# Kernel tuning notes

Hardware: AMD Instinct MI355X
Metric: run time of the kernel (lower is better)

Reference implementation:

```python
import jax, jax.numpy as jnp
import numpy as np

B, L, D, H = 65536, 20, 4, 1024
T = 61  # output_length; 60 RK4 steps


def setup_inputs() -> dict:
    key = jax.random.key(0)
    ks = jax.random.split(key, 16)
    # small positive states so the quadratic SEIR dynamics stay finite over 60 steps
    xx = jax.random.uniform(ks[0], (B, L, D), dtype=jnp.float32) * 0.1
    dims = [L * D] + [H] * 6 + [3]
    inp = {"xx": xx}
    for i in range(7):
        scale = 1.0 / np.sqrt(dims[i])
        W = jax.random.normal(ks[1 + 2 * i], (dims[i], dims[i + 1]), dtype=jnp.float32) * scale
        if i == 6:
            W = W * 1e-3  # keep beta/gamma/sigma small -> stable integration
        inp[f"W{i}"] = W
        inp[f"b{i}"] = jnp.zeros((dims[i + 1],), jnp.float32)
    inp["output_length"] = T
    return inp


def reference(xx, W0, b0, W1, b1, W2, b2, W3, b3, W4, b4, W5, b5, W6, b6, output_length):
    h = xx.reshape(xx.shape[0], -1)  # (B, L*D)
    for W, b in ((W0, b0), (W1, b1), (W2, b2), (W3, b3), (W4, b4), (W5, b5)):
        h = jax.nn.leaky_relu(h @ W + b, negative_slope=0.01)
    out = h @ W6 + b6  # (B, 3)
    beta, gamma, sigma = out[:, 0:1], out[:, 1:2], out[:, 2:3]  # each (B,1)

    initial = xx[:, 0]  # (B, 4) = S,E,I,R at t0
    S0, E0, I0, R0 = (initial[:, i:i + 1] for i in range(4))
    # self.step = 1 in the torch module, so dt is folded in as 1.0

    def derivs(S, E, I):
        SI = beta * S * I
        return -SI, SI - sigma * E, sigma * E - gamma * I, gamma * I

    def body(carry, _):
        S, E, I, R = carry
        k1S, k1E, k1I, k1R = derivs(S, E, I)
        k2S, k2E, k2I, k2R = derivs(S + 0.5 * k1S, E + 0.5 * k1E, I + 0.5 * k1I)
        k3S, k3E, k3I, k3R = derivs(S + 0.5 * k2S, E + 0.5 * k2E, I + 0.5 * k2I)
        k4S, k4E, k4I, k4R = derivs(S + k3S, E + k3E, I + k3I)
        upd = lambda f, k1, k2, k3, k4: f + (k1 + 2 * k2 + 2 * k3 + k4) / 6.0
        new = (upd(S, k1S, k2S, k3S, k4S),
               upd(E, k1E, k2E, k3E, k4E),
               upd(I, k1I, k2I, k3I, k4I),
               upd(R, k1R, k2R, k3R, k4R))
        return new, jnp.concatenate(new, axis=1)  # (B,4) per step

    _, ys = jax.lax.scan(body, (S0, E0, I0, R0), None, length=output_length - 1)
    y0 = jnp.concatenate([S0, E0, I0, R0], axis=1)  # (B,4)
    y = jnp.concatenate([y0[None], ys], axis=0)     # (T,B,4)
    return jnp.transpose(y, (1, 0, 2))              # (B,T,4) in S,E,I,R order
```

## Files before the change

kernel.cpp:

```cpp
#include <hip/hip_runtime.h>
#include <stdint.h>

typedef short s16x8 __attribute__((ext_vector_type(8)));
typedef __bf16 bf16x8 __attribute__((ext_vector_type(8)));
typedef float f32x4 __attribute__((ext_vector_type(4)));

typedef const __attribute__((address_space(1))) void* gas_ptr;
typedef __attribute__((address_space(3))) void* las_ptr;

__device__ __forceinline__ unsigned short f2bf(float f) {
  unsigned u = __builtin_bit_cast(unsigned, f);
  u += 0x7FFFu + ((u >> 16) & 1u);
  return (unsigned short)(u >> 16);
}
__device__ __forceinline__ float bf2f(unsigned short h) {
  return __builtin_bit_cast(float, (unsigned)h << 16);
}
__device__ __forceinline__ void async16(const void* g, void* l) {
  __builtin_amdgcn_global_load_lds((gas_ptr)g, (las_ptr)l, 16, 0, 0);
}

__global__ void prep_x0(const float* __restrict__ xx, unsigned short* __restrict__ X0,
                        int rowOffset, int rows) {
  int idx = blockIdx.x * blockDim.x + threadIdx.x;
  if (idx >= rows * 128) return;
  int r = idx >> 7, c = idx & 127;
  float v = (c < 80) ? xx[(size_t)(rowOffset + r) * 80 + c] : 0.f;
  X0[(size_t)r * 128 + c] = f2bf(v);
}

struct TP {
  const float* W[6];
  unsigned short* WT[6];
  const float* xx;
  unsigned short* X0;
  int prepRows;
};

__global__ void prep_all(TP tp) {
  const int z = blockIdx.z;
  const int tx = threadIdx.x, ty = threadIdx.y;
  if (z == 6) {
    const long long total = (long long)tp.prepRows * 128;
    long long i = ((long long)(blockIdx.y * 32 + blockIdx.x) * 256) + (ty * 32 + tx);
    for (; i < total; i += 262144) {
      const int r = (int)(i >> 7), c = (int)(i & 127);
      float v = (c < 80) ? tp.xx[(size_t)r * 80 + c] : 0.f;
      tp.X0[(size_t)r * 128 + c] = f2bf(v);
    }
    return;
  }
  const int K  = (z == 0) ? 80  : 1024;
  const int KP = (z == 0) ? 128 : 1024;
  if (blockIdx.y * 32 >= KP) return;
  __shared__ float tile[32][33];
  const int n0 = blockIdx.x * 32, k0 = blockIdx.y * 32;
  const float* W = tp.W[z];
  unsigned short* WT = tp.WT[z];
  #pragma unroll
  for (int j = 0; j < 32; j += 8) {
    int k = k0 + ty + j;
    tile[ty + j][tx] = (k < K) ? W[(size_t)k * 1024 + n0 + tx] : 0.f;
  }
  __syncthreads();
  #pragma unroll
  for (int j = 0; j < 32; j += 8) {
    WT[(size_t)(n0 + ty + j) * KP + k0 + tx] = f2bf(tile[tx][ty + j]);
  }
}

#define BM 128
#define BN 128
#define BK 64

__global__ void gemm_mlp(const unsigned short* __restrict__ A,
                         const unsigned short* __restrict__ BT,
                         const float* __restrict__ bias,
                         unsigned short* __restrict__ C,
                         int M, int N, int K, int leaky) {
  __shared__ unsigned short As[BM * BK];
  __shared__ unsigned short Bs[BN * BK];

  const int tid  = threadIdx.x;
  const int wid  = tid >> 6;
  const int lane = tid & 63;
  const int wr = (wid >> 1) * 64;
  const int wc = (wid & 1) * 64;
  const int bn = blockIdx.x * BN;
  const int bm = blockIdx.y * BM;

  const int srow = lane >> 3;
  const int scol = (lane & 7) * 8;

  f32x4 acc[4][4] = {};

  const unsigned short* aTile = A  + (size_t)bm * K;
  const unsigned short* bTile = BT + (size_t)bn * K;

  for (int k0 = 0; k0 < K; k0 += BK) {
    #pragma unroll
    for (int j = 0; j < 4; ++j) {
      const int rg = wid + j * 4;
      async16(aTile + (size_t)(rg * 8 + srow) * K + k0 + scol, &As[rg * 8 * BK]);
      async16(bTile + (size_t)(rg * 8 + srow) * K + k0 + scol, &Bs[rg * 8 * BK]);
    }
    __syncthreads();

    const int fr = lane & 15;
    const int kq = (lane >> 4) * 8;
    #pragma unroll
    for (int ks = 0; ks < BK; ks += 32) {
      const int kk = ks + kq;
      bf16x8 af[4], bv[4];
      #pragma unroll
      for (int m = 0; m < 4; ++m)
        af[m] = __builtin_bit_cast(bf16x8, *(const s16x8*)&As[(wr + m * 16 + fr) * BK + kk]);
      #pragma unroll
      for (int n = 0; n < 4; ++n)
        bv[n] = __builtin_bit_cast(bf16x8, *(const s16x8*)&Bs[(wc + n * 16 + fr) * BK + kk]);
      #pragma unroll
      for (int m = 0; m < 4; ++m)
        #pragma unroll
        for (int n = 0; n < 4; ++n)
          acc[m][n] = __builtin_amdgcn_mfma_f32_16x16x32_bf16(af[m], bv[n], acc[m][n], 0, 0, 0);
    }
    __syncthreads();
  }

  const int fcol = lane & 15;
  const int frow = (lane >> 4) * 4;
  #pragma unroll
  for (int m = 0; m < 4; ++m) {
    #pragma unroll
    for (int n = 0; n < 4; ++n) {
      const int col = bn + wc + n * 16 + fcol;
      const float bb = bias[col];
      #pragma unroll
      for (int r = 0; r < 4; ++r) {
        const int row = bm + wr + m * 16 + frow + r;
        float v = acc[m][n][r] + bb;
        if (leaky) v = (v > 0.f) ? v : 0.01f * v;
        C[(size_t)row * N + col] = f2bf(v);
      }
    }
  }
}


__device__ __forceinline__ void stage_half(const char* srcRow0, size_t ldb,
                                           char* ldsHalf, int w, int rsub, int usw) {
  #pragma unroll
  for (int l = 0; l < 2; ++l) {
    const char* src = srcRow0 + (size_t)((l * 8 + w) * 8 + rsub) * ldb + usw;
    async16(src, ldsHalf + (l * 8 + w) * 1024);
  }
}

#define MFMA16 __builtin_amdgcn_mfma_f32_16x16x32_bf16
#define EPAD 72
#define EBYTES (64 * EPAD * 2)

template <int HEAD>
__global__ __launch_bounds__(512, 2)
void gemm8(const unsigned short* __restrict__ A,
           const unsigned short* __restrict__ BT,
           const float* __restrict__ bias,
           unsigned short* __restrict__ C,
           const float* __restrict__ W6,
           float* __restrict__ partial,
           int M, int N, int K) {
  extern __shared__ char smem[];
  char* smA = smem;
  char* smB = smem + 65536;
  const unsigned short* sA = (const unsigned short*)smA;
  const unsigned short* sB = (const unsigned short*)smB;
  const int NTk = K >> 6;

  const int tid  = threadIdx.x;
  const int w    = tid >> 6;
  const int lane = tid & 63;

  const int nwg = gridDim.x;
  const int bid = blockIdx.x;
  const int q = nwg >> 3, r = nwg & 7;
  const int xcd = bid & 7, idx = bid >> 3;
  const int wg = (xcd < r ? xcd * (q + 1) : r * (q + 1) + (xcd - r) * q) + idx;
  const int nNT = N >> 8;
  const int mtile = wg / nNT, ntile = wg % nNT;
  const int bm = mtile << 8, bn = ntile << 8;

  const int wr = (w >> 2) << 7;
  const int wc = (w & 3) << 6;
  const int fr = lane & 15;
  const int e0 = lane >> 4;
  const int sw = lane & 7;
  const int rsub = lane >> 3;
  const int usw  = ((sw ^ rsub) << 4);
  const int col0 = (((e0)     ^ sw) << 3);
  const int col1 = (((e0 + 4) ^ sw) << 3);
  const int fcol = lane & 15;

  const size_t ldb = (size_t)K * 2;
  const char* Ab = (const char*)A  + (size_t)bm * ldb;
  const char* Bb = (const char*)BT + (size_t)bn * ldb;

  f32x4 acc[8][4] = {};

#define RDA(c_, row_, col_) __builtin_bit_cast(bf16x8, *(const s16x8*)&sA[(c_) * 16384 + (row_) * 64 + (col_)])
#define RDB(c_, row_, col_) __builtin_bit_cast(bf16x8, *(const s16x8*)&sB[(c_) * 16384 + (row_) * 64 + (col_)])

  stage_half(Bb,                    ldb, smB,                  w, rsub, usw);
  stage_half(Bb + 128 * ldb,        ldb, smB + 16384,          w, rsub, usw);
  stage_half(Ab,                    ldb, smA,                  w, rsub, usw);
  stage_half(Ab + 128 * ldb,        ldb, smA + 16384,          w, rsub, usw);
  stage_half(Bb + 128,              ldb, smB + 32768,          w, rsub, usw);
  stage_half(Bb + 128 * ldb + 128,  ldb, smB + 32768 + 16384,  w, rsub, usw);
  asm volatile("s_waitcnt vmcnt(4)" ::: "memory");
  __builtin_amdgcn_s_barrier();

  for (int kt = 0; kt < NTk; ++kt) {
    const int c = kt & 1;
    bf16x8 aF[4][2], bF[4][2];

    #pragma unroll
    for (int m = 0; m < 4; ++m) {
      const int row = wr + m * 16 + fr;
      aF[m][0] = RDA(c, row, col0);
      aF[m][1] = RDA(c, row, col1);
    }
    #pragma unroll
    for (int n = 0; n < 2; ++n) {
      const int row = wc + n * 16 + fr;
      bF[n][0] = RDB(c, row, col0);
      bF[n][1] = RDB(c, row, col1);
    }
    if (kt + 1 < NTk)
      stage_half(Ab + (size_t)(kt + 1) * 128, ldb, smA + (c ^ 1) * 32768, w, rsub, usw);
    __builtin_amdgcn_s_barrier();
    __builtin_amdgcn_s_setprio(1);
    #pragma unroll
    for (int m = 0; m < 4; ++m)
      #pragma unroll
      for (int n = 0; n < 2; ++n) {
        acc[m][n] = MFMA16(aF[m][0], bF[n][0], acc[m][n], 0, 0, 0);
        acc[m][n] = MFMA16(aF[m][1], bF[n][1], acc[m][n], 0, 0, 0);
      }
    __builtin_amdgcn_s_setprio(0);
    __builtin_amdgcn_s_barrier();

    #pragma unroll
    for (int n = 2; n < 4; ++n) {
      const int row = wc + n * 16 + fr;
      bF[n][0] = RDB(c, row, col0);
      bF[n][1] = RDB(c, row, col1);
    }
    if (kt + 1 < NTk)
      stage_half(Ab + 128 * ldb + (size_t)(kt + 1) * 128, ldb,
                 smA + (c ^ 1) * 32768 + 16384, w, rsub, usw);
    __builtin_amdgcn_s_barrier();
    __builtin_amdgcn_s_setprio(1);
    #pragma unroll
    for (int m = 0; m < 4; ++m)
      #pragma unroll
      for (int n = 2; n < 4; ++n) {
        acc[m][n] = MFMA16(aF[m][0], bF[n][0], acc[m][n], 0, 0, 0);
        acc[m][n] = MFMA16(aF[m][1], bF[n][1], acc[m][n], 0, 0, 0);
      }
    __builtin_amdgcn_s_setprio(0);
    __builtin_amdgcn_s_barrier();

    #pragma unroll
    for (int m = 0; m < 4; ++m) {
      const int row = wr + (m + 4) * 16 + fr;
      aF[m][0] = RDA(c, row, col0);
      aF[m][1] = RDA(c, row, col1);
    }
    if (kt + 2 < NTk)
      stage_half(Bb + (size_t)(kt + 2) * 128, ldb, smB + c * 32768, w, rsub, usw);
    __builtin_amdgcn_s_barrier();
    __builtin_amdgcn_s_setprio(1);
    #pragma unroll
    for (int m = 0; m < 4; ++m)
      #pragma unroll
      for (int n = 0; n < 2; ++n) {
        acc[m + 4][n] = MFMA16(aF[m][0], bF[n][0], acc[m + 4][n], 0, 0, 0);
        acc[m + 4][n] = MFMA16(aF[m][1], bF[n][1], acc[m + 4][n], 0, 0, 0);
      }
    __builtin_amdgcn_s_setprio(0);
    __builtin_amdgcn_s_barrier();

    if (kt + 2 < NTk)
      stage_half(Bb + 128 * ldb + (size_t)(kt + 2) * 128, ldb,
                 smB + c * 32768 + 16384, w, rsub, usw);
    __builtin_amdgcn_s_barrier();
    __builtin_amdgcn_s_setprio(1);
    #pragma unroll
    for (int m = 0; m < 4; ++m)
      #pragma unroll
      for (int n = 2; n < 4; ++n) {
        acc[m + 4][n] = MFMA16(aF[m][0], bF[n][0], acc[m + 4][n], 0, 0, 0);
        acc[m + 4][n] = MFMA16(aF[m][1], bF[n][1], acc[m + 4][n], 0, 0, 0);
      }
    __builtin_amdgcn_s_setprio(0);
    if (kt + 2 < NTk) asm volatile("s_waitcnt vmcnt(4)" ::: "memory");
    else              asm volatile("s_waitcnt vmcnt(0)" ::: "memory");
    __builtin_amdgcn_s_barrier();
  }

#undef RDA
#undef RDB

  float bbv[4];
  #pragma unroll
  for (int n = 0; n < 4; ++n) bbv[n] = bias[bn + wc + n * 16 + fcol];

  if constexpr (HEAD) {
    float w6c[4][3];
    #pragma unroll
    for (int n = 0; n < 4; ++n) {
      const int col = bn + wc + n * 16 + fcol;
      #pragma unroll
      for (int j = 0; j < 3; ++j) w6c[n][j] = W6[col * 3 + j];
    }
    const int nt = bn >> 8;
    #pragma unroll
    for (int mh = 0; mh < 2; ++mh)
      #pragma unroll
      for (int mm = 0; mm < 4; ++mm)
        #pragma unroll
        for (int rr = 0; rr < 4; ++rr) {
          float s0 = 0.f, s1 = 0.f, s2 = 0.f;
          #pragma unroll
          for (int n = 0; n < 4; ++n) {
            float v = acc[mh * 4 + mm][n][rr] + bbv[n];
            v = (v > 0.f) ? v : 0.01f * v;
            s0 = fmaf(v, w6c[n][0], s0);
            s1 = fmaf(v, w6c[n][1], s1);
            s2 = fmaf(v, w6c[n][2], s2);
          }
          #pragma unroll
          for (int off = 1; off < 16; off <<= 1) {
            s0 += __shfl_xor(s0, off);
            s1 += __shfl_xor(s1, off);
            s2 += __shfl_xor(s2, off);
          }
          if (fcol == 0) {
            const int row = bm + wr + mh * 64 + mm * 16 + e0 * 4 + rr;
            *(float4*)&partial[((size_t)nt * M + row) * 4] =
                make_float4(s0, s1, s2, 0.f);
          }
        }
  } else {
    unsigned short* eb = (unsigned short*)(smem + w * EBYTES);
    const int r8 = lane >> 3, c8 = (lane & 7) * 8;
    #pragma unroll
    for (int mh = 0; mh < 2; ++mh) {
      #pragma unroll
      for (int mm = 0; mm < 4; ++mm)
        #pragma unroll
        for (int n = 0; n < 4; ++n)
          #pragma unroll
          for (int rr = 0; rr < 4; ++rr) {
            const int row64 = mm * 16 + e0 * 4 + rr;
            float v = acc[mh * 4 + mm][n][rr] + bbv[n];
            v = (v > 0.f) ? v : 0.01f * v;
            eb[row64 * EPAD + n * 16 + fcol] = f2bf(v);
          }
      asm volatile("" ::: "memory");
      #pragma unroll
      for (int rg = 0; rg < 8; ++rg) {
        const int row64 = rg * 8 + r8;
        s16x8 vv = *(const s16x8*)&eb[row64 * EPAD + c8];
        const int rl = bm + wr + mh * 64 + row64;
        *(s16x8*)&C[(size_t)rl * N + bn + wc + c8] = vv;
      }
      asm volatile("" ::: "memory");
    }
  }
}

__global__ void rk4_traj(const float* __restrict__ partial,
                         const float* __restrict__ b6,
                         const float* __restrict__ xx,
                         float* __restrict__ out,
                         int rowOffset, int rows, int T) {
  const int r = blockIdx.x * blockDim.x + threadIdx.x;
  if (r >= rows) return;
  const size_t grow = (size_t)rowOffset + r;

  float4 p0 = *(const float4*)&partial[((size_t)0 * rows + r) * 4];
  float4 p1 = *(const float4*)&partial[((size_t)1 * rows + r) * 4];
  float4 p2 = *(const float4*)&partial[((size_t)2 * rows + r) * 4];
  float4 p3 = *(const float4*)&partial[((size_t)3 * rows + r) * 4];
  const float beta  = p0.x + p1.x + p2.x + p3.x + b6[0];
  const float gamma = p0.y + p1.y + p2.y + p3.y + b6[1];
  const float sigma = p0.z + p1.z + p2.z + p3.z + b6[2];

  const float4 iv = *(const float4*)(xx + grow * 80);
  float S = iv.x, E = iv.y, I = iv.z, R = iv.w;
  float* o = out + grow * (size_t)T * 4;
  *(float4*)o = iv;

#define DERIVS(S_, E_, I_, dS, dE, dI, dR)      \
  {                                             \
    float SI = beta * (S_) * (I_);              \
    float sE = sigma * (E_);                    \
    float gI = gamma * (I_);                    \
    dS = -SI; dE = SI - sE; dI = sE - gI; dR = gI; \
  }

  for (int t = 1; t < T; ++t) {
    float k1S, k1E, k1I, k1R; DERIVS(S, E, I, k1S, k1E, k1I, k1R);
    float k2S, k2E, k2I, k2R; DERIVS(S + 0.5f * k1S, E + 0.5f * k1E, I + 0.5f * k1I, k2S, k2E, k2I, k2R);
    float k3S, k3E, k3I, k3R; DERIVS(S + 0.5f * k2S, E + 0.5f * k2E, I + 0.5f * k2I, k3S, k3E, k3I, k3R);
    float k4S, k4E, k4I, k4R; DERIVS(S + k3S, E + k3E, I + k3I, k4S, k4E, k4I, k4R);
    S += (k1S + 2.f * k2S + 2.f * k3S + k4S) * (1.f / 6.f);
    E += (k1E + 2.f * k2E + 2.f * k3E + k4E) * (1.f / 6.f);
    I += (k1I + 2.f * k2I + 2.f * k3I + k4I) * (1.f / 6.f);
    R += (k1R + 2.f * k2R + 2.f * k3R + k4R) * (1.f / 6.f);
    *(float4*)(o + (size_t)t * 4) = make_float4(S, E, I, R);
  }
#undef DERIVS
}

extern "C" void kernel_launch(void* const* d_in, const int* in_sizes, int n_in,
                              void* d_out, int out_size, void* d_ws, size_t ws_size,
                              hipStream_t stream) {
  const float* xx = (const float*)d_in[0];
  const float* W[7];
  const float* bb[7];
  for (int i = 0; i < 7; ++i) {
    W[i]  = (const float*)d_in[1 + 2 * i];
    bb[i] = (const float*)d_in[2 + 2 * i];
  }
  const int B = in_sizes[0] / 80;
  const int T = out_size / (B * 4);
  float* out = (float*)d_out;

  {
    auto k0 = gemm8<0>;
    auto k1 = gemm8<1>;
    hipFuncSetAttribute((const void*)k0, hipFuncAttributeMaxDynamicSharedMemorySize, 131072);
    hipFuncSetAttribute((const void*)k1, hipFuncAttributeMaxDynamicSharedMemorySize, 131072);
  }

  uint8_t* ws = (uint8_t*)d_ws;
  size_t off = 0;
  auto alloc = [&](size_t bytes) -> uint8_t* {
    uint8_t* p = ws + off;
    off += (bytes + 255) & ~(size_t)255;
    return p;
  };

  unsigned short* WTl[6];
  WTl[0] = (unsigned short*)alloc((size_t)1024 * 128 * 2);
  for (int i = 1; i < 6; ++i) WTl[i] = (unsigned short*)alloc((size_t)1024 * 1024 * 2);

  const size_t weightBytes = off;
  const size_t avail = ws_size > weightBytes ? ws_size - weightBytes : 0;
  int Bc = (int)(avail / 4416);
  Bc = (Bc / 256) * 256;
  if (Bc > B) Bc = B;
  if (Bc < 256) Bc = 256;
  const bool fullBatch = (Bc >= B);

  unsigned short* X0   = (unsigned short*)alloc((size_t)Bc * 128 * 2);
  unsigned short* buf0 = (unsigned short*)alloc((size_t)Bc * 1024 * 2);
  unsigned short* buf1 = (unsigned short*)alloc((size_t)Bc * 1024 * 2);
  float* partial       = (float*)alloc((size_t)Bc * 4 * 16);

  {
    TP tp;
    for (int i = 0; i < 6; ++i) { tp.W[i] = W[i]; tp.WT[i] = WTl[i]; }
    tp.xx = xx;
    tp.X0 = X0;
    tp.prepRows = fullBatch ? B : 0;
    prep_all<<<dim3(32, 32, 7), dim3(32, 8), 0, stream>>>(tp);
  }

  for (int r0 = 0; r0 < B; r0 += Bc) {
    const int rows = (B - r0 < Bc) ? (B - r0) : Bc;

    if (!fullBatch) {
      const int n = rows * 128;
      prep_x0<<<(n + 255) / 256, 256, 0, stream>>>(xx, X0, r0, rows);
    }

    gemm_mlp<<<dim3(8, rows / 128), 256, 0, stream>>>(X0, WTl[0], bb[0], buf0,
                                                      rows, 1024, 128, 1);

    const int nwg = (rows / 256) * 4;
    gemm8<0><<<nwg, 512, 131072, stream>>>(buf0, WTl[1], bb[1], buf1, nullptr, nullptr, rows, 1024, 1024);
    gemm8<0><<<nwg, 512, 131072, stream>>>(buf1, WTl[2], bb[2], buf0, nullptr, nullptr, rows, 1024, 1024);
    gemm8<0><<<nwg, 512, 131072, stream>>>(buf0, WTl[3], bb[3], buf1, nullptr, nullptr, rows, 1024, 1024);
    gemm8<0><<<nwg, 512, 131072, stream>>>(buf1, WTl[4], bb[4], buf0, nullptr, nullptr, rows, 1024, 1024);

    gemm8<1><<<nwg, 512, 131072, stream>>>(buf0, WTl[5], bb[5], nullptr, W[6], partial, rows, 1024, 1024);

    rk4_traj<<<(rows + 255) / 256, 256, 0, stream>>>(partial, bb[6], xx, out, r0, rows, T);
  }
}
```

Measured before the change: 963.6 us.

## Fuse RK4 trajectory into last GEMM via atomic last-block counter

Removes the separate rk4_traj kernel. Each M-tile in the final layer's GEMM bumps an atomic counter, and the last of the four N-tile workgroups to finish sums the partials and runs the RK4 integration in-kernel. This saves a kernel launch and the partial-buffer round trip, and lets the integration overlap with other GEMM tiles. The cost is atomic synchronisation and RK4 work on only 256 of 512 threads in the finishing block, with a counter reset per tile.

After: 1.038 ms. 7.7% more time.

```diff
diff --git a/kernel.cpp b/kernel.cpp
--- a/kernel.cpp
+++ b/kernel.cpp
@@ -34,6 +34,7 @@
   unsigned short* WT[6];
   const float* xx;
   unsigned short* X0;
+  unsigned* cnt;
   int prepRows;
 };
 
@@ -41,6 +42,10 @@
   const int z = blockIdx.z;
   const int tx = threadIdx.x, ty = threadIdx.y;
   if (z == 6) {
+    if (blockIdx.x == 0 && blockIdx.y == 0) {
+      const int t = ty * 32 + tx;
+      if (t < 256) tp.cnt[t] = 0;
+    }
     const long long total = (long long)tp.prepRows * 128;
     long long i = ((long long)(blockIdx.y * 32 + blockIdx.x) * 256) + (ty * 32 + tx);
     for (; i < total; i += 262144) {
@@ -168,6 +173,11 @@
            unsigned short* __restrict__ C,
            const float* __restrict__ W6,
            float* __restrict__ partial,
+           unsigned* __restrict__ cnt,
+           const float* __restrict__ xx,
+           const float* __restrict__ b6,
+           float* __restrict__ out,
+           int rowOffset, int T,
            int M, int N, int K) {
   extern __shared__ char smem[];
   char* smA = smem;
@@ -346,10 +356,59 @@
           }
           if (fcol == 0) {
             const int row = bm + wr + mh * 64 + mm * 16 + e0 * 4 + rr;
-            *(float4*)&partial[((size_t)nt * M + row) * 4] =
-                make_float4(s0, s1, s2, 0.f);
+            float* p = &partial[((size_t)nt * M + row) * 4];
+            __hip_atomic_store(p + 0, s0, __ATOMIC_RELAXED, __HIP_MEMORY_SCOPE_AGENT);
+            __hip_atomic_store(p + 1, s1, __ATOMIC_RELAXED, __HIP_MEMORY_SCOPE_AGENT);
+            __hip_atomic_store(p + 2, s2, __ATOMIC_RELAXED, __HIP_MEMORY_SCOPE_AGENT);
           }
         }
+
+    __syncthreads();
+    unsigned* sh = (unsigned*)smem;
+    if (tid == 0)
+      sh[0] = __hip_atomic_fetch_add(&cnt[mtile], 1u, __ATOMIC_ACQ_REL,
+                                     __HIP_MEMORY_SCOPE_AGENT);
+    __syncthreads();
+    if (sh[0] == 3u) {
+      if (tid < 256) {
+        const int row = bm + tid;
+        float pv0 = 0.f, pv1 = 0.f, pv2 = 0.f;
+        #pragma unroll
+        for (int nt2 = 0; nt2 < 4; ++nt2) {
+          const float* p = &partial[((size_t)nt2 * M + row) * 4];
+          pv0 += __hip_atomic_load(p + 0, __ATOMIC_RELAXED, __HIP_MEMORY_SCOPE_AGENT);
+          pv1 += __hip_atomic_load(p + 1, __ATOMIC_RELAXED, __HIP_MEMORY_SCOPE_AGENT);
+          pv2 += __hip_atomic_load(p + 2, __ATOMIC_RELAXED, __HIP_MEMORY_SCOPE_AGENT);
+        }
+        const float beta = pv0 + b6[0], gamma = pv1 + b6[1], sigma = pv2 + b6[2];
+        const size_t grow = (size_t)rowOffset + row;
+        const float4 iv = *(const float4*)(xx + grow * 80);
+        float S = iv.x, E = iv.y, I = iv.z, R = iv.w;
+        float* o = out + grow * (size_t)T * 4;
+        *(float4*)o = iv;
+#define DERIVS(S_, E_, I_, dS, dE, dI, dR)         \
+        {                                          \
+          float SI = beta * (S_) * (I_);           \
+          float sE = sigma * (E_);                 \
+          float gI = gamma * (I_);                 \
+          dS = -SI; dE = SI - sE; dI = sE - gI; dR = gI; \
+        }
+        for (int t = 1; t < T; ++t) {
+          float k1S, k1E, k1I, k1R; DERIVS(S, E, I, k1S, k1E, k1I, k1R);
+          float k2S, k2E, k2I, k2R; DERIVS(S + 0.5f * k1S, E + 0.5f * k1E, I + 0.5f * k1I, k2S, k2E, k2I, k2R);
+          float k3S, k3E, k3I, k3R; DERIVS(S + 0.5f * k2S, E + 0.5f * k2E, I + 0.5f * k2I, k3S, k3E, k3I, k3R);
+          float k4S, k4E, k4I, k4R; DERIVS(S + k3S, E + k3E, I + k3I, k4S, k4E, k4I, k4R);
+          S += (k1S + 2.f * k2S + 2.f * k3S + k4S) * (1.f / 6.f);
+          E += (k1E + 2.f * k2E + 2.f * k3E + k4E) * (1.f / 6.f);
+          I += (k1I + 2.f * k2I + 2.f * k3I + k4I) * (1.f / 6.f);
+          R += (k1R + 2.f * k2R + 2.f * k3R + k4R) * (1.f / 6.f);
+          *(float4*)(o + (size_t)t * 4) = make_float4(S, E, I, R);
+        }
+#undef DERIVS
+      }
+      if (tid == 0)
+        __hip_atomic_store(&cnt[mtile], 0u, __ATOMIC_RELAXED, __HIP_MEMORY_SCOPE_AGENT);
+    }
   } else {
     unsigned short* eb = (unsigned short*)(smem + w * EBYTES);
     const int r8 = lane >> 3, c8 = (lane & 7) * 8;
@@ -379,50 +438,6 @@
   }
 }
 
-__global__ void rk4_traj(const float* __restrict__ partial,
-                         const float* __restrict__ b6,
-                         const float* __restrict__ xx,
-                         float* __restrict__ out,
-                         int rowOffset, int rows, int T) {
-  const int r = blockIdx.x * blockDim.x + threadIdx.x;
-  if (r >= rows) return;
-  const size_t grow = (size_t)rowOffset + r;
-
-  float4 p0 = *(const float4*)&partial[((size_t)0 * rows + r) * 4];
-  float4 p1 = *(const float4*)&partial[((size_t)1 * rows + r) * 4];
-  float4 p2 = *(const float4*)&partial[((size_t)2 * rows + r) * 4];
-  float4 p3 = *(const float4*)&partial[((size_t)3 * rows + r) * 4];
-  const float beta  = p0.x + p1.x + p2.x + p3.x + b6[0];
-  const float gamma = p0.y + p1.y + p2.y + p3.y + b6[1];
-  const float sigma = p0.z + p1.z + p2.z + p3.z + b6[2];
-
-  const float4 iv = *(const float4*)(xx + grow * 80);
-  float S = iv.x, E = iv.y, I = iv.z, R = iv.w;
-  float* o = out + grow * (size_t)T * 4;
-  *(float4*)o = iv;
-
-#define DERIVS(S_, E_, I_, dS, dE, dI, dR)      \
-  {                                             \
-    float SI = beta * (S_) * (I_);              \
-    float sE = sigma * (E_);                    \
-    float gI = gamma * (I_);                    \
-    dS = -SI; dE = SI - sE; dI = sE - gI; dR = gI; \
-  }
-
-  for (int t = 1; t < T; ++t) {
-    float k1S, k1E, k1I, k1R; DERIVS(S, E, I, k1S, k1E, k1I, k1R);
-    float k2S, k2E, k2I, k2R; DERIVS(S + 0.5f * k1S, E + 0.5f * k1E, I + 0.5f * k1I, k2S, k2E, k2I, k2R);
-    float k3S, k3E, k3I, k3R; DERIVS(S + 0.5f * k2S, E + 0.5f * k2E, I + 0.5f * k2I, k3S, k3E, k3I, k3R);
-    float k4S, k4E, k4I, k4R; DERIVS(S + k3S, E + k3E, I + k3I, k4S, k4E, k4I, k4R);
-    S += (k1S + 2.f * k2S + 2.f * k3S + k4S) * (1.f / 6.f);
-    E += (k1E + 2.f * k2E + 2.f * k3E + k4E) * (1.f / 6.f);
-    I += (k1I + 2.f * k2I + 2.f * k3I + k4I) * (1.f / 6.f);
-    R += (k1R + 2.f * k2R + 2.f * k3R + k4R) * (1.f / 6.f);
-    *(float4*)(o + (size_t)t * 4) = make_float4(S, E, I, R);
-  }
-#undef DERIVS
-}
-
 extern "C" void kernel_launch(void* const* d_in, const int* in_sizes, int n_in,
                               void* d_out, int out_size, void* d_ws, size_t ws_size,
                               hipStream_t stream) {
@@ -455,6 +470,7 @@
   unsigned short* WTl[6];
   WTl[0] = (unsigned short*)alloc((size_t)1024 * 128 * 2);
   for (int i = 1; i < 6; ++i) WTl[i] = (unsigned short*)alloc((size_t)1024 * 1024 * 2);
+  unsigned* cnt = (unsigned*)alloc(256 * sizeof(unsigned));
 
   const size_t weightBytes = off;
   const size_t avail = ws_size > weightBytes ? ws_size - weightBytes : 0;
@@ -474,6 +490,7 @@
     for (int i = 0; i < 6; ++i) { tp.W[i] = W[i]; tp.WT[i] = WTl[i]; }
     tp.xx = xx;
     tp.X0 = X0;
+    tp.cnt = cnt;
     tp.prepRows = fullBatch ? B : 0;
     prep_all<<<dim3(32, 32, 7), dim3(32, 8), 0, stream>>>(tp);
   }
@@ -490,13 +507,21 @@
                                                       rows, 1024, 128, 1);
 
     const int nwg = (rows / 256) * 4;
-    gemm8<0><<<nwg, 512, 131072, stream>>>(buf0, WTl[1], bb[1], buf1, nullptr, nullptr, rows, 1024, 1024);
-    gemm8<0><<<nwg, 512, 131072, stream>>>(buf1, WTl[2], bb[2], buf0, nullptr, nullptr, rows, 1024, 1024);
-    gemm8<0><<<nwg, 512, 131072, stream>>>(buf0, WTl[3], bb[3], buf1, nullptr, nullptr, rows, 1024, 1024);
-    gemm8<0><<<nwg, 512, 131072, stream>>>(buf1, WTl[4], bb[4], buf0, nullptr, nullptr, rows, 1024, 1024);
-
-    gemm8<1><<<nwg, 512, 131072, stream>>>(buf0, WTl[5], bb[5], nullptr, W[6], partial, rows, 1024, 1024);
-
-    rk4_traj<<<(rows + 255) / 256, 256, 0, stream>>>(partial, bb[6], xx, out, r0, rows, T);
-  }
-}
+    gemm8<0><<<nwg, 512, 131072, stream>>>(buf0, WTl[1], bb[1], buf1, nullptr, nullptr,
+                                           nullptr, nullptr, nullptr, nullptr, 0, 0,
+                                           rows, 1024, 1024);
+    gemm8<0><<<nwg, 512, 131072, stream>>>(buf1, WTl[2], bb[2], buf0, nullptr, nullptr,
+                                           nullptr, nullptr, nullptr, nullptr, 0, 0,
+                                           rows, 1024, 1024);
+    gemm8<0><<<nwg, 512, 131072, stream>>>(buf0, WTl[3], bb[3], buf1, nullptr, nullptr,
+                                           nullptr, nullptr, nullptr, nullptr, 0, 0,
+                                           rows, 1024, 1024);
+    gemm8<0><<<nwg, 512, 131072, stream>>>(buf1, WTl[4], bb[4], buf0, nullptr, nullptr,
+                                           nullptr, nullptr, nullptr, nullptr, 0, 0,
+                                           rows, 1024, 1024);
+
+    gemm8<1><<<nwg, 512, 131072, stream>>>(buf0, WTl[5], bb[5], nullptr, W[6], partial,
+                                           cnt, xx, bb[6], out, r0, T,
+                                           rows, 1024, 1024);
+  }
+}
```

## Fuse final MLP layer, output head and RK4 integration into one kernel

Applied to the files above, without the earlier changes.

Replaces the templated head GEMM plus separate rk4_traj kernel with a gemm8_head kernel where each workgroup owns a 256-row M tile and loops over all four N tiles. The 3-wide head partial sums go into extra LDS, are reduced per row, and the RK4 trajectory is integrated and written out in the same kernel. This removes the global partial buffer and one launch. The cost is that the last GEMM launches a quarter as many workgroups, each doing four times the work, so parallelism and occupancy on that layer drop (extra LDS also raises per-block shared memory).

After: 1.066 ms. 1.11x slower.

```diff
diff --git a/kernel.cpp b/kernel.cpp
--- a/kernel.cpp
+++ b/kernel.cpp
@@ -160,14 +160,108 @@
 #define EPAD 72
 #define EBYTES (64 * EPAD * 2)
 
-template <int HEAD>
+#define GEMM8_KLOOP                                                              \
+  stage_half(Bb,                    ldb, smB,                  w, rsub, usw);    \
+  stage_half(Bb + 128 * ldb,        ldb, smB + 16384,          w, rsub, usw);    \
+  stage_half(Ab,                    ldb, smA,                  w, rsub, usw);    \
+  stage_half(Ab + 128 * ldb,        ldb, smA + 16384,          w, rsub, usw);    \
+  stage_half(Bb + 128,              ldb, smB + 32768,          w, rsub, usw);    \
+  stage_half(Bb + 128 * ldb + 128,  ldb, smB + 32768 + 16384,  w, rsub, usw);    \
+  asm volatile("s_waitcnt vmcnt(4)" ::: "memory");                               \
+  __builtin_amdgcn_s_barrier();                                                  \
+  for (int kt = 0; kt < NTk; ++kt) {                                             \
+    const int c = kt & 1;                                                        \
+    bf16x8 aF[4][2], bF[4][2];                                                   \
+    _Pragma("unroll")                                                            \
+    for (int m = 0; m < 4; ++m) {                                                \
+      const int row = wr + m * 16 + fr;                                          \
+      aF[m][0] = RDA(c, row, col0);                                              \
+      aF[m][1] = RDA(c, row, col1);                                              \
+    }                                                                            \
+    _Pragma("unroll")                                                            \
+    for (int n = 0; n < 2; ++n) {                                                \
+      const int row = wc + n * 16 + fr;                                          \
+      bF[n][0] = RDB(c, row, col0);                                              \
+      bF[n][1] = RDB(c, row, col1);                                              \
+    }                                                                            \
+    if (kt + 1 < NTk)                                                            \
+      stage_half(Ab + (size_t)(kt + 1) * 128, ldb, smA + (c ^ 1) * 32768, w, rsub, usw); \
+    __builtin_amdgcn_s_barrier();                                                \
+    __builtin_amdgcn_s_setprio(1);                                               \
+    _Pragma("unroll")                                                            \
+    for (int m = 0; m < 4; ++m)                                                  \
+      _Pragma("unroll")                                                          \
+      for (int n = 0; n < 2; ++n) {                                              \
+        acc[m][n] = MFMA16(aF[m][0], bF[n][0], acc[m][n], 0, 0, 0);              \
+        acc[m][n] = MFMA16(aF[m][1], bF[n][1], acc[m][n], 0, 0, 0);              \
+      }                                                                          \
+    __builtin_amdgcn_s_setprio(0);                                               \
+    __builtin_amdgcn_s_barrier();                                                \
+    _Pragma("unroll")                                                            \
+    for (int n = 2; n < 4; ++n) {                                                \
+      const int row = wc + n * 16 + fr;                                          \
+      bF[n][0] = RDB(c, row, col0);                                              \
+      bF[n][1] = RDB(c, row, col1);                                              \
+    }                                                                            \
+    if (kt + 1 < NTk)                                                            \
+      stage_half(Ab + 128 * ldb + (size_t)(kt + 1) * 128, ldb,                   \
+                 smA + (c ^ 1) * 32768 + 16384, w, rsub, usw);                   \
+    __builtin_amdgcn_s_barrier();                                                \
+    __builtin_amdgcn_s_setprio(1);                                               \
+    _Pragma("unroll")                                                            \
+    for (int m = 0; m < 4; ++m)                                                  \
+      _Pragma("unroll")                                                          \
+      for (int n = 2; n < 4; ++n) {                                              \
+        acc[m][n] = MFMA16(aF[m][0], bF[n][0], acc[m][n], 0, 0, 0);              \
+        acc[m][n] = MFMA16(aF[m][1], bF[n][1], acc[m][n], 0, 0, 0);              \
+      }                                                                          \
+    __builtin_amdgcn_s_setprio(0);                                               \
+    __builtin_amdgcn_s_barrier();                                                \
+    _Pragma("unroll")                                                            \
+    for (int m = 0; m < 4; ++m) {                                                \
+      const int row = wr + (m + 4) * 16 + fr;                                    \
+      aF[m][0] = RDA(c, row, col0);                                              \
+      aF[m][1] = RDA(c, row, col1);                                              \
+    }                                                                            \
+    if (kt + 2 < NTk)                                                            \
+      stage_half(Bb + (size_t)(kt + 2) * 128, ldb, smB + c * 32768, w, rsub, usw); \
+    __builtin_amdgcn_s_barrier();                                                \
+    __builtin_amdgcn_s_setprio(1);                                               \
+    _Pragma("unroll")                                                            \
+    for (int m = 0; m < 4; ++m)                                                  \
+      _Pragma("unroll")                                                          \
+      for (int n = 0; n < 2; ++n) {                                              \
+        acc[m + 4][n] = MFMA16(aF[m][0], bF[n][0], acc[m + 4][n], 0, 0, 0);      \
+        acc[m + 4][n] = MFMA16(aF[m][1], bF[n][1], acc[m + 4][n], 0, 0, 0);      \
+      }                                                                          \
+    __builtin_amdgcn_s_setprio(0);                                               \
+    __builtin_amdgcn_s_barrier();                                                \
+    if (kt + 2 < NTk)                                                            \
+      stage_half(Bb + 128 * ldb + (size_t)(kt + 2) * 128, ldb,                   \
+                 smB + c * 32768 + 16384, w, rsub, usw);                         \
+    __builtin_amdgcn_s_barrier();                                                \
+    __builtin_amdgcn_s_setprio(1);                                               \
+    _Pragma("unroll")                                                            \
+    for (int m = 0; m < 4; ++m)                                                  \
+      _Pragma("unroll")                                                          \
+      for (int n = 2; n < 4; ++n) {                                              \
+        acc[m + 4][n] = MFMA16(aF[m][0], bF[n][0], acc[m + 4][n], 0, 0, 0);      \
+        acc[m + 4][n] = MFMA16(aF[m][1], bF[n][1], acc[m + 4][n], 0, 0, 0);      \
+      }                                                                          \
+    __builtin_amdgcn_s_setprio(0);                                               \
+    if (kt + 2 < NTk) asm volatile("s_waitcnt vmcnt(4)" ::: "memory");           \
+    else              asm volatile("s_waitcnt vmcnt(0)" ::: "memory");           \
+    __builtin_amdgcn_s_barrier();                                                \
+  }
+
+#define RDA(c_, row_, col_) __builtin_bit_cast(bf16x8, *(const s16x8*)&sA[(c_) * 16384 + (row_) * 64 + (col_)])
+#define RDB(c_, row_, col_) __builtin_bit_cast(bf16x8, *(const s16x8*)&sB[(c_) * 16384 + (row_) * 64 + (col_)])
+
 __global__ __launch_bounds__(512, 2)
 void gemm8(const unsigned short* __restrict__ A,
            const unsigned short* __restrict__ BT,
            const float* __restrict__ bias,
            unsigned short* __restrict__ C,
-           const float* __restrict__ W6,
-           float* __restrict__ partial,
            int M, int N, int K) {
   extern __shared__ char smem[];
   char* smA = smem;
@@ -206,123 +300,100 @@
 
   f32x4 acc[8][4] = {};
 
-#define RDA(c_, row_, col_) __builtin_bit_cast(bf16x8, *(const s16x8*)&sA[(c_) * 16384 + (row_) * 64 + (col_)])
-#define RDB(c_, row_, col_) __builtin_bit_cast(bf16x8, *(const s16x8*)&sB[(c_) * 16384 + (row_) * 64 + (col_)])
-
-  stage_half(Bb,                    ldb, smB,                  w, rsub, usw);
-  stage_half(Bb + 128 * ldb,        ldb, smB + 16384,          w, rsub, usw);
-  stage_half(Ab,                    ldb, smA,                  w, rsub, usw);
-  stage_half(Ab + 128 * ldb,        ldb, smA + 16384,          w, rsub, usw);
-  stage_half(Bb + 128,              ldb, smB + 32768,          w, rsub, usw);
-  stage_half(Bb + 128 * ldb + 128,  ldb, smB + 32768 + 16384,  w, rsub, usw);
-  asm volatile("s_waitcnt vmcnt(4)" ::: "memory");
-  __builtin_amdgcn_s_barrier();
-
-  for (int kt = 0; kt < NTk; ++kt) {
-    const int c = kt & 1;
-    bf16x8 aF[4][2], bF[4][2];
-
-    #pragma unroll
-    for (int m = 0; m < 4; ++m) {
-      const int row = wr + m * 16 + fr;
-      aF[m][0] = RDA(c, row, col0);
-      aF[m][1] = RDA(c, row, col1);
-    }
-    #pragma unroll
-    for (int n = 0; n < 2; ++n) {
-      const int row = wc + n * 16 + fr;
-      bF[n][0] = RDB(c, row, col0);
-      bF[n][1] = RDB(c, row, col1);
-    }
-    if (kt + 1 < NTk)
-      stage_half(Ab + (size_t)(kt + 1) * 128, ldb, smA + (c ^ 1) * 32768, w, rsub, usw);
-    __builtin_amdgcn_s_barrier();
-    __builtin_amdgcn_s_setprio(1);
-    #pragma unroll
-    for (int m = 0; m < 4; ++m)
-      #pragma unroll
-      for (int n = 0; n < 2; ++n) {
-        acc[m][n] = MFMA16(aF[m][0], bF[n][0], acc[m][n], 0, 0, 0);
-        acc[m][n] = MFMA16(aF[m][1], bF[n][1], acc[m][n], 0, 0, 0);
-      }
-    __builtin_amdgcn_s_setprio(0);
-    __builtin_amdgcn_s_barrier();
-
-    #pragma unroll
-    for (int n = 2; n < 4; ++n) {
-      const int row = wc + n * 16 + fr;
-      bF[n][0] = RDB(c, row, col0);
-      bF[n][1] = RDB(c, row, col1);
-    }
-    if (kt + 1 < NTk)
-      stage_half(Ab + 128 * ldb + (size_t)(kt + 1) * 128, ldb,
-                 smA + (c ^ 1) * 32768 + 16384, w, rsub, usw);
-    __builtin_amdgcn_s_barrier();
-    __builtin_amdgcn_s_setprio(1);
-    #pragma unroll
-    for (int m = 0; m < 4; ++m)
-      #pragma unroll
-      for (int n = 2; n < 4; ++n) {
-        acc[m][n] = MFMA16(aF[m][0], bF[n][0], acc[m][n], 0, 0, 0);
-        acc[m][n] = MFMA16(aF[m][1], bF[n][1], acc[m][n], 0, 0, 0);
-      }
-    __builtin_amdgcn_s_setprio(0);
-    __builtin_amdgcn_s_barrier();
-
-    #pragma unroll
-    for (int m = 0; m < 4; ++m) {
-      const int row = wr + (m + 4) * 16 + fr;
-      aF[m][0] = RDA(c, row, col0);
-      aF[m][1] = RDA(c, row, col1);
-    }
-    if (kt + 2 < NTk)
-      stage_half(Bb + (size_t)(kt + 2) * 128, ldb, smB + c * 32768, w, rsub, usw);
-    __builtin_amdgcn_s_barrier();
-    __builtin_amdgcn_s_setprio(1);
-    #pragma unroll
-    for (int m = 0; m < 4; ++m)
-      #pragma unroll
-      for (int n = 0; n < 2; ++n) {
-        acc[m + 4][n] = MFMA16(aF[m][0], bF[n][0], acc[m + 4][n], 0, 0, 0);
-        acc[m + 4][n] = MFMA16(aF[m][1], bF[n][1], acc[m + 4][n], 0, 0, 0);
-      }
-    __builtin_amdgcn_s_setprio(0);
-    __builtin_amdgcn_s_barrier();
-
-    if (kt + 2 < NTk)
-      stage_half(Bb + 128 * ldb + (size_t)(kt + 2) * 128, ldb,
-                 smB + c * 32768 + 16384, w, rsub, usw);
-    __builtin_amdgcn_s_barrier();
-    __builtin_amdgcn_s_setprio(1);
-    #pragma unroll
-    for (int m = 0; m < 4; ++m)
-      #pragma unroll
-      for (int n = 2; n < 4; ++n) {
-        acc[m + 4][n] = MFMA16(aF[m][0], bF[n][0], acc[m + 4][n], 0, 0, 0);
-        acc[m + 4][n] = MFMA16(aF[m][1], bF[n][1], acc[m + 4][n], 0, 0, 0);
-      }
-    __builtin_amdgcn_s_setprio(0);
-    if (kt + 2 < NTk) asm volatile("s_waitcnt vmcnt(4)" ::: "memory");
-    else              asm volatile("s_waitcnt vmcnt(0)" ::: "memory");
-    __builtin_amdgcn_s_barrier();
-  }
-
-#undef RDA
-#undef RDB
+  GEMM8_KLOOP
 
   float bbv[4];
   #pragma unroll
   for (int n = 0; n < 4; ++n) bbv[n] = bias[bn + wc + n * 16 + fcol];
 
-  if constexpr (HEAD) {
+  unsigned short* eb = (unsigned short*)(smem + w * EBYTES);
+  const int r8 = lane >> 3, c8 = (lane & 7) * 8;
+  #pragma unroll
+  for (int mh = 0; mh < 2; ++mh) {
+    #pragma unroll
+    for (int mm = 0; mm < 4; ++mm)
+      #pragma unroll
+      for (int n = 0; n < 4; ++n)
+        #pragma unroll
+        for (int rr = 0; rr < 4; ++rr) {
+          const int row64 = mm * 16 + e0 * 4 + rr;
+          float v = acc[mh * 4 + mm][n][rr] + bbv[n];
+          v = (v > 0.f) ? v : 0.01f * v;
+          eb[row64 * EPAD + n * 16 + fcol] = f2bf(v);
+        }
+    asm volatile("" ::: "memory");
+    #pragma unroll
+    for (int rg = 0; rg < 8; ++rg) {
+      const int row64 = rg * 8 + r8;
+      s16x8 vv = *(const s16x8*)&eb[row64 * EPAD + c8];
+      const int rl = bm + wr + mh * 64 + row64;
+      *(s16x8*)&C[(size_t)rl * N + bn + wc + c8] = vv;
+    }
+    asm volatile("" ::: "memory");
+  }
+}
+
+__global__ __launch_bounds__(512, 2)
+void gemm8_head(const unsigned short* __restrict__ A,
+                const unsigned short* __restrict__ BT,
+                const float* __restrict__ bias,
+                const float* __restrict__ W6,
+                const float* __restrict__ b6,
+                const float* __restrict__ xx,
+                float* __restrict__ out,
+                int rowOffset, int T,
+                int M, int N, int K) {
+  extern __shared__ char smem[];
+  char* smA = smem;
+  char* smB = smem + 65536;
+  float* hsum = (float*)(smem + 131072);
+  const unsigned short* sA = (const unsigned short*)smA;
+  const unsigned short* sB = (const unsigned short*)smB;
+  const int NTk = K >> 6;
+
+  const int tid  = threadIdx.x;
+  const int w    = tid >> 6;
+  const int lane = tid & 63;
+
+  const int nwg = gridDim.x;
+  const int bid = blockIdx.x;
+  const int q = nwg >> 3, r = nwg & 7;
+  const int xcd = bid & 7, idx = bid >> 3;
+  const int mtile = (xcd < r ? xcd * (q + 1) : r * (q + 1) + (xcd - r) * q) + idx;
+  const int bm = mtile << 8;
+
+  const int wr = (w >> 2) << 7;
+  const int wc = (w & 3) << 6;
+  const int fr = lane & 15;
+  const int e0 = lane >> 4;
+  const int sw = lane & 7;
+  const int rsub = lane >> 3;
+  const int usw  = ((sw ^ rsub) << 4);
+  const int col0 = (((e0)     ^ sw) << 3);
+  const int col1 = (((e0 + 4) ^ sw) << 3);
+  const int fcol = lane & 15;
+
+  const size_t ldb = (size_t)K * 2;
+  const char* Ab = (const char*)A + (size_t)bm * ldb;
+
+  for (int nt = 0; nt < 4; ++nt) {
+    const int bn = nt << 8;
+    const char* Bb = (const char*)BT + (size_t)bn * ldb;
+
+    f32x4 acc[8][4] = {};
+
+    GEMM8_KLOOP
+
+    float bbv[4];
     float w6c[4][3];
     #pragma unroll
     for (int n = 0; n < 4; ++n) {
       const int col = bn + wc + n * 16 + fcol;
+      bbv[n] = bias[col];
       #pragma unroll
       for (int j = 0; j < 3; ++j) w6c[n][j] = W6[col * 3 + j];
     }
-    const int nt = bn >> 8;
+
     #pragma unroll
     for (int mh = 0; mh < 2; ++mh)
       #pragma unroll
@@ -345,83 +416,53 @@
             s2 += __shfl_xor(s2, off);
           }
           if (fcol == 0) {
-            const int row = bm + wr + mh * 64 + mm * 16 + e0 * 4 + rr;
-            *(float4*)&partial[((size_t)nt * M + row) * 4] =
-                make_float4(s0, s1, s2, 0.f);
+            const int row = wr + mh * 64 + mm * 16 + e0 * 4 + rr;
+            float* p = &hsum[(nt * 256 + row) * 3];
+            p[0] = s0; p[1] = s1; p[2] = s2;
           }
         }
-  } else {
-    unsigned short* eb = (unsigned short*)(smem + w * EBYTES);
-    const int r8 = lane >> 3, c8 = (lane & 7) * 8;
-    #pragma unroll
-    for (int mh = 0; mh < 2; ++mh) {
-      #pragma unroll
-      for (int mm = 0; mm < 4; ++mm)
-        #pragma unroll
-        for (int n = 0; n < 4; ++n)
-          #pragma unroll
-          for (int rr = 0; rr < 4; ++rr) {
-            const int row64 = mm * 16 + e0 * 4 + rr;
-            float v = acc[mh * 4 + mm][n][rr] + bbv[n];
-            v = (v > 0.f) ? v : 0.01f * v;
-            eb[row64 * EPAD + n * 16 + fcol] = f2bf(v);
-          }
-      asm volatile("" ::: "memory");
-      #pragma unroll
-      for (int rg = 0; rg < 8; ++rg) {
-        const int row64 = rg * 8 + r8;
-        s16x8 vv = *(const s16x8*)&eb[row64 * EPAD + c8];
-        const int rl = bm + wr + mh * 64 + row64;
-        *(s16x8*)&C[(size_t)rl * N + bn + wc + c8] = vv;
-      }
-      asm volatile("" ::: "memory");
-    }
-  }
-}
-
-__global__ void rk4_traj(const float* __restrict__ partial,
-                         const float* __restrict__ b6,
-                         const float* __restrict__ xx,
-                         float* __restrict__ out,
-                         int rowOffset, int rows, int T) {
-  const int r = blockIdx.x * blockDim.x + threadIdx.x;
-  if (r >= rows) return;
-  const size_t grow = (size_t)rowOffset + r;
-
-  float4 p0 = *(const float4*)&partial[((size_t)0 * rows + r) * 4];
-  float4 p1 = *(const float4*)&partial[((size_t)1 * rows + r) * 4];
-  float4 p2 = *(const float4*)&partial[((size_t)2 * rows + r) * 4];
-  float4 p3 = *(const float4*)&partial[((size_t)3 * rows + r) * 4];
-  const float beta  = p0.x + p1.x + p2.x + p3.x + b6[0];
-  const float gamma = p0.y + p1.y + p2.y + p3.y + b6[1];
-  const float sigma = p0.z + p1.z + p2.z + p3.z + b6[2];
-
-  const float4 iv = *(const float4*)(xx + grow * 80);
-  float S = iv.x, E = iv.y, I = iv.z, R = iv.w;
-  float* o = out + grow * (size_t)T * 4;
-  *(float4*)o = iv;
-
-#define DERIVS(S_, E_, I_, dS, dE, dI, dR)      \
-  {                                             \
-    float SI = beta * (S_) * (I_);              \
-    float sE = sigma * (E_);                    \
-    float gI = gamma * (I_);                    \
-    dS = -SI; dE = SI - sE; dI = sE - gI; dR = gI; \
-  }
-
-  for (int t = 1; t < T; ++t) {
-    float k1S, k1E, k1I, k1R; DERIVS(S, E, I, k1S, k1E, k1I, k1R);
-    float k2S, k2E, k2I, k2R; DERIVS(S + 0.5f * k1S, E + 0.5f * k1E, I + 0.5f * k1I, k2S, k2E, k2I, k2R);
-    float k3S, k3E, k3I, k3R; DERIVS(S + 0.5f * k2S, E + 0.5f * k2E, I + 0.5f * k2I, k3S, k3E, k3I, k3R);
-    float k4S, k4E, k4I, k4R; DERIVS(S + k3S, E + k3E, I + k3I, k4S, k4E, k4I, k4R);
-    S += (k1S + 2.f * k2S + 2.f * k3S + k4S) * (1.f / 6.f);
-    E += (k1E + 2.f * k2E + 2.f * k3E + k4E) * (1.f / 6.f);
-    I += (k1I + 2.f * k2I + 2.f * k3I + k4I) * (1.f / 6.f);
-    R += (k1R + 2.f * k2R + 2.f * k3R + k4R) * (1.f / 6.f);
-    *(float4*)(o + (size_t)t * 4) = make_float4(S, E, I, R);
-  }
+  }
+
+  __syncthreads();
+
+  if (tid < 256) {
+    const int row = tid;
+    float pv0 = 0.f, pv1 = 0.f, pv2 = 0.f;
+    #pragma unroll
+    for (int nt = 0; nt < 4; ++nt) {
+      const float* p = &hsum[(nt * 256 + row) * 3];
+      pv0 += p[0]; pv1 += p[1]; pv2 += p[2];
+    }
+    const float beta = pv0 + b6[0], gamma = pv1 + b6[1], sigma = pv2 + b6[2];
+    const size_t grow = (size_t)rowOffset + bm + row;
+    const float4 iv = *(const float4*)(xx + grow * 80);
+    float S = iv.x, E = iv.y, I = iv.z, R = iv.w;
+    float* o = out + grow * (size_t)T * 4;
+    *(float4*)o = iv;
+#define DERIVS(S_, E_, I_, dS, dE, dI, dR)         \
+    {                                              \
+      float SI = beta * (S_) * (I_);               \
+      float sE = sigma * (E_);                     \
+      float gI = gamma * (I_);                     \
+      dS = -SI; dE = SI - sE; dI = sE - gI; dR = gI; \
+    }
+    for (int t = 1; t < T; ++t) {
+      float k1S, k1E, k1I, k1R; DERIVS(S, E, I, k1S, k1E, k1I, k1R);
+      float k2S, k2E, k2I, k2R; DERIVS(S + 0.5f * k1S, E + 0.5f * k1E, I + 0.5f * k1I, k2S, k2E, k2I, k2R);
+      float k3S, k3E, k3I, k3R; DERIVS(S + 0.5f * k2S, E + 0.5f * k2E, I + 0.5f * k2I, k3S, k3E, k3I, k3R);
+      float k4S, k4E, k4I, k4R; DERIVS(S + k3S, E + k3E, I + k3I, k4S, k4E, k4I, k4R);
+      S += (k1S + 2.f * k2S + 2.f * k3S + k4S) * (1.f / 6.f);
+      E += (k1E + 2.f * k2E + 2.f * k3E + k4E) * (1.f / 6.f);
+      I += (k1I + 2.f * k2I + 2.f * k3I + k4I) * (1.f / 6.f);
+      R += (k1R + 2.f * k2R + 2.f * k3R + k4R) * (1.f / 6.f);
+      *(float4*)(o + (size_t)t * 4) = make_float4(S, E, I, R);
+    }
 #undef DERIVS
-}
+  }
+}
+
+#undef RDA
+#undef RDB
 
 extern "C" void kernel_launch(void* const* d_in, const int* in_sizes, int n_in,
                               void* d_out, int out_size, void* d_ws, size_t ws_size,
@@ -437,12 +478,10 @@
   const int T = out_size / (B * 4);
   float* out = (float*)d_out;
 
-  {
-    auto k0 = gemm8<0>;
-    auto k1 = gemm8<1>;
-    hipFuncSetAttribute((const void*)k0, hipFuncAttributeMaxDynamicSharedMemorySize, 131072);
-    hipFuncSetAttribute((const void*)k1, hipFuncAttributeMaxDynamicSharedMemorySize, 131072);
-  }
+  hipFuncSetAttribute((const void*)gemm8,
+                      hipFuncAttributeMaxDynamicSharedMemorySize, 131072);
+  hipFuncSetAttribute((const void*)gemm8_head,
+                      hipFuncAttributeMaxDynamicSharedMemorySize, 143360);
 
   uint8_t* ws = (uint8_t*)d_ws;
   size_t off = 0;
@@ -458,7 +497,7 @@
 
   const size_t weightBytes = off;
   const size_t avail = ws_size > weightBytes ? ws_size - weightBytes : 0;
-  int Bc = (int)(avail / 4416);
+  int Bc = (int)(avail / 4352);
   Bc = (Bc / 256) * 256;
   if (Bc > B) Bc = B;
   if (Bc < 256) Bc = 256;
@@ -467,7 +506,6 @@
   unsigned short* X0   = (unsigned short*)alloc((size_t)Bc * 128 * 2);
   unsigned short* buf0 = (unsigned short*)alloc((size_t)Bc * 1024 * 2);
   unsigned short* buf1 = (unsigned short*)alloc((size_t)Bc * 1024 * 2);
-  float* partial       = (float*)alloc((size_t)Bc * 4 * 16);
 
   {
     TP tp;
@@ -490,13 +528,12 @@
                                                       rows, 1024, 128, 1);
 
     const int nwg = (rows / 256) * 4;
-    gemm8<0><<<nwg, 512, 131072, stream>>>(buf0, WTl[1], bb[1], buf1, nullptr, nullptr, rows, 1024, 1024);
-    gemm8<0><<<nwg, 512, 131072, stream>>>(buf1, WTl[2], bb[2], buf0, nullptr, nullptr, rows, 1024, 1024);
-    gemm8<0><<<nwg, 512, 131072, stream>>>(buf0, WTl[3], bb[3], buf1, nullptr, nullptr, rows, 1024, 1024);
-    gemm8<0><<<nwg, 512, 131072, stream>>>(buf1, WTl[4], bb[4], buf0, nullptr, nullptr, rows, 1024, 1024);
-
-    gemm8<1><<<nwg, 512, 131072, stream>>>(buf0, WTl[5], bb[5], nullptr, W[6], partial, rows, 1024, 1024);
-
-    rk4_traj<<<(rows + 255) / 256, 256, 0, stream>>>(partial, bb[6], xx, out, r0, rows, T);
-  }
-}
+    gemm8<<<nwg, 512, 131072, stream>>>(buf0, WTl[1], bb[1], buf1, rows, 1024, 1024);
+    gemm8<<<nwg, 512, 131072, stream>>>(buf1, WTl[2], bb[2], buf0, rows, 1024, 1024);
+    gemm8<<<nwg, 512, 131072, stream>>>(buf0, WTl[3], bb[3], buf1, rows, 1024, 1024);
+    gemm8<<<nwg, 512, 131072, stream>>>(buf1, WTl[4], bb[4], buf0, rows, 1024, 1024);
+
+    gemm8_head<<<rows / 256, 512, 143360, stream>>>(buf0, WTl[5], bb[5], W[6], bb[6],
+                                                    xx, out, r0, T, rows, 1024, 1024);
+  }
+}
```
